# Kernel optimization log

Hardware: AMD Instinct MI355X
Metric: run time of the kernel (lower is better)

The kernel has to match this reference:

```python
import jax, jax.numpy as jnp
import numpy as np

K = 30  # hardcoded top-k in take_top_k_dropout(x, 30, ...)


def _topk_channel_mask(x, k):
    # x: [B, C, H, W]; binary mask with 1 at the top-k |x| channels per pixel.
    B, C, H, W = x.shape
    xa = jnp.abs(x).reshape(B, C, H * W).transpose(0, 2, 1).reshape(B * H * W, C)
    _, idx = jax.lax.top_k(xa, k)  # [BHW, k]
    rows = jnp.arange(B * H * W)[:, None]
    mask = jnp.zeros((B * H * W, C), x.dtype).at[rows, idx].set(1.0)
    return mask.reshape(B, H * W, C).transpose(0, 2, 1).reshape(B, C, H, W)


def _saturation(z, phi, jump):
    # Saturation_activation_per_filter.forward
    l1 = (jnp.sum(jnp.abs(phi), axis=0) + 1e-12).reshape(1, -1, 1, 1)  # [1,C,1,1]
    r = z / l1
    r = 0.5 * (jnp.sign(r - jump) + jnp.sign(r + jump))
    return r * l1


def _conv_transpose(x, w, b, stride):
    # PyTorch ConvTranspose2d(padding=0): w is [in, out, kh, kw]
    k = w.shape[-1]
    wt = jnp.flip(w, (2, 3)).transpose(1, 0, 2, 3)  # -> [out, in, kh, kw]
    y = jax.lax.conv_general_dilated(
        x, wt, window_strides=(1, 1),
        padding=[(k - 1, k - 1), (k - 1, k - 1)],
        lhs_dilation=(stride, stride),
        dimension_numbers=('NCHW', 'OIHW', 'NCHW'))
    return y + b.reshape(1, -1, 1, 1)


def _take_middle(x):
    width = x.shape[-1]
    s = (width - 32) // 2
    return x[:, :, s:s + 32, s:s + 32]


def setup_inputs() -> dict:
    key = jax.random.key(0)
    ks = jax.random.split(key, 9)
    B, C, H, W, D = 128, 500, 16, 16, 192
    return {
        'x': jax.random.normal(ks[0], (B, C, H, W), jnp.float32),
        'phi': jax.random.normal(ks[1], (D, C), jnp.float32),
        'jump': jnp.float32(0.1),
        'w1': jax.random.normal(ks[2], (C, 300, 4, 4), jnp.float32) * 0.02,
        'b1': jax.random.normal(ks[3], (300,), jnp.float32) * 0.02,
        'w2': jax.random.normal(ks[4], (300, 100, 3, 3), jnp.float32) * 0.02,
        'b2': jax.random.normal(ks[5], (100,), jnp.float32) * 0.02,
        'w3': jax.random.normal(ks[6], (100, 3, 3, 3), jnp.float32) * 0.02,
        'b3': jax.random.normal(ks[7], (3,), jnp.float32) * 0.02,
    }


def reference(x, phi, jump, w1, b1, w2, b2, w3, b3):
    # eval mode: dropout(ones) == ones, no training rescalings
    out = x * _topk_channel_mask(x, K)
    out = _saturation(out, phi, jump)
    out = jax.nn.relu(_conv_transpose(out, w1, b1, 2))
    out = jax.nn.relu(_conv_transpose(out, w2, b2, 1))
    out = jax.nn.relu(_conv_transpose(out, w3, b3, 1))
    return _take_middle(out)
```

## Files before the change

### kernel.cpp

```cpp
#include <hip/hip_runtime.h>
#include <stdint.h>

#define B_   128
#define C_   500
#define H_   16
#define P_   256
#define D_   192
#define C1O  300
#define H1   34
#define P1   (H1*H1)
#define C2O  100
#define H2   36
#define P2   (H2*H2)
#define C3O  3
#define H3   38
#define P3   (H3*H3)
#define CROP 3
#define OW_  32
#define KTOP 30

#define NL1B   16
#define NZQBLK (B_ * 4)
#define NB3BLK ((P3 + 3) / 4)

__device__ __forceinline__ float sgnf(float v){ return (v > 0.f) ? 1.f : ((v < 0.f) ? -1.f : 0.f); }

__device__ __forceinline__ int pat36(int i){
  if (i == 0) return 0;
  if (i == 1) return 1;
  if (i <= 33) return 2;
  if (i == 34) return 3;
  return 4;
}

__global__ void k_setup(const float* __restrict__ phi, const float* __restrict__ jumpp,
                        const float* __restrict__ w2, const float* __restrict__ b1,
                        const float* __restrict__ b2,
                        float* __restrict__ l1, float* __restrict__ thr,
                        float* __restrict__ tab, float4* __restrict__ zero_region){
  const int blk = blockIdx.x;
  const int t = threadIdx.x;

  if (blk >= NL1B + 100){
    const int idx0 = (blk - (NL1B + 100)) * 256 + t;
    const int nvec = (16 + B_ * P1 + B_ * P2) / 16;
    float4 z = make_float4(0.f, 0.f, 0.f, 0.f);
    for (int i = idx0; i < nvec; i += 64 * 256) zero_region[i] = z;
    return;
  }

  if (blk < NL1B){
    __shared__ float red[8][32];
    const int cl = t & 31, dg = t >> 5;
    const int c = blk * 32 + cl;
    float s = 0.f;
    if (c < C_){
      const int d0 = dg * 24;
#pragma unroll 4
      for (int d = d0; d < d0 + 24; ++d) s += fabsf(phi[d * C_ + c]);
    }
    red[dg][cl] = s;
    __syncthreads();
    if (t < 32){
      int cc = blk * 32 + t;
      if (cc < C_){
        float sum = 1e-12f;
#pragma unroll
        for (int g = 0; g < 8; ++g) sum += red[g][t];
        l1[cc] = sum;
        thr[cc] = jumpp[0] * sum;
      }
    }
    return;
  }

  __shared__ float S[9];
  const int o = blk - NL1B;
  if (t < 64){
    float acc[9] = {0,0,0,0,0,0,0,0,0};
    for (int c = t; c < C1O; c += 64){
      float a1 = fmaxf(b1[c], 0.f);
      const float* w = w2 + (c * C2O + o) * 9;
#pragma unroll
      for (int tap = 0; tap < 9; ++tap) acc[tap] += w[tap] * a1;
    }
#pragma unroll
    for (int tap = 0; tap < 9; ++tap)
      for (int off = 32; off; off >>= 1) acc[tap] += __shfl_down(acc[tap], off);
    if (t == 0){
#pragma unroll
      for (int tap = 0; tap < 9; ++tap) S[tap] = acc[tap];
    }
  }
  __syncthreads();
  if (t < 25){
    const int lo[5] = {0,0,0,1,2}, hi[5] = {0,1,2,2,2};
    int pr = t / 5, pc = t % 5;
    float s = b2[o];
    for (int kh = lo[pr]; kh <= hi[pr]; ++kh)
      for (int kw = lo[pc]; kw <= hi[pc]; ++kw) s += S[kh * 3 + kw];
    tab[o * 25 + t] = s;
  }
}

__global__ void k_zq_b3(const float* __restrict__ x, const float* __restrict__ l1,
                        const float* __restrict__ thr, const float* __restrict__ jumpp,
                        const float* __restrict__ tab, const float* __restrict__ w3,
                        const float* __restrict__ b3,
                        signed char* __restrict__ zq, unsigned char* __restrict__ d0,
                        float* __restrict__ base3, int* __restrict__ cnt){
  if (blockIdx.x >= NZQBLK){
    const int wave = threadIdx.x >> 6, lane = threadIdx.x & 63;
    const int pix = (blockIdx.x - NZQBLK) * 4 + wave;
    if (pix >= P3) return;
    const int oh = pix / H3, ow = pix % H3;
    float acc[3] = {0, 0, 0};
    for (int c = lane; c < C2O; c += 64){
      const float* w = w3 + c * 27;
#pragma unroll
      for (int kh = 0; kh < 3; ++kh){
        int ih = oh - kh; if (ih < 0 || ih >= H2) continue;
        int prr = pat36(ih) * 5;
#pragma unroll
        for (int kw = 0; kw < 3; ++kw){
          int iw = ow - kw; if (iw < 0 || iw >= H2) continue;
          float a2 = fmaxf(tab[c * 25 + prr + pat36(iw)], 0.f);
#pragma unroll
          for (int o = 0; o < 3; ++o) acc[o] += w[o * 9 + kh * 3 + kw] * a2;
        }
      }
    }
#pragma unroll
    for (int o = 0; o < 3; ++o){
      for (int off = 32; off; off >>= 1) acc[o] += __shfl_down(acc[o], off);
    }
    if (lane == 0){
#pragma unroll
      for (int o = 0; o < 3; ++o) base3[o * P3 + pix] = acc[o] + b3[o];
    }
    return;
  }

  const int b = blockIdx.x >> 2;
  const int tile = (blockIdx.x & 3) * 64;
  const int t = threadIdx.x;
  const int q = t & 15, cg = t >> 4;

  __shared__ unsigned char um[256];
  __shared__ unsigned char pixf[64];
  __shared__ int s_any;
  if (t == 0) s_any = 0;

  unsigned m = 0;
  const int pbase = tile + 4 * q;
  for (int c = cg; c < C_; c += 16){
    float tc = thr[c];
    const float4 v = *(const float4*)(x + ((size_t)(b * C_ + c)) * P_ + pbase);
    if (fabsf(v.x) >= tc) m |= 1u;
    if (fabsf(v.y) >= tc) m |= 2u;
    if (fabsf(v.z) >= tc) m |= 4u;
    if (fabsf(v.w) >= tc) m |= 8u;
  }
  um[t] = (unsigned char)m;
  __syncthreads();
  if (t < 16){
    unsigned mm = 0;
#pragma unroll
    for (int g = 0; g < 16; ++g) mm |= um[g * 16 + t];
#pragma unroll
    for (int j = 0; j < 4; ++j){
      unsigned char f = (unsigned char)((mm >> j) & 1u);
      pixf[4 * t + j] = f;
      d0[b * P_ + tile + 4 * t + j] = f;
    }
    if (mm) s_any = 1;
  }
  __syncthreads();
  if (t == 0 && s_any) atomicAdd(cnt, 1);
  if (!s_any) return;

  __shared__ float sx[C_];
  __shared__ unsigned char rm[C_];
  __shared__ unsigned long long red[4];
  __shared__ int sel[KTOP];
  float J = jumpp[0];
  for (int pp = 0; pp < 64; ++pp){
    if (!pixf[pp]) continue;
    int px = tile + pp;
    for (int c = t; c < C_; c += 256){ sx[c] = x[(b * C_ + c) * P_ + px]; rm[c] = 0; }
    __syncthreads();
    for (int it = 0; it < KTOP; ++it){
      unsigned long long best = 0ULL;
      for (int c = t; c < C_; c += 256){
        if (!rm[c]){
          unsigned long long key =
            ((unsigned long long)__float_as_uint(fabsf(sx[c])) << 32) |
            (unsigned int)(C_ - 1 - c);
          if (key > best) best = key;
        }
      }
      for (int off = 32; off; off >>= 1){
        unsigned long long o2 = __shfl_down(best, off);
        if (o2 > best) best = o2;
      }
      if ((t & 63) == 0) red[t >> 6] = best;
      __syncthreads();
      if (t == 0){
        unsigned long long mx = red[0];
        for (int wv = 1; wv < 4; ++wv) if (red[wv] > mx) mx = red[wv];
        int idx = C_ - 1 - (int)(mx & 0xffffffffULL);
        sel[it] = idx;
        rm[idx] = 1;
      }
      __syncthreads();
    }
    for (int c = t; c < C_; c += 256) zq[(b * C_ + c) * P_ + px] = 0;
    __syncthreads();
    if (t < KTOP){
      int c = sel[t];
      float z = sx[c];
      float r = z / l1[c];
      float qv = 0.5f * (sgnf(r - J) + sgnf(r + J));
      int code = (int)(2.f * qv);
      if (code) zq[(b * C_ + c) * P_ + px] = (signed char)code;
    }
    __syncthreads();
  }
}

__global__ void k_u1f(const signed char* __restrict__ zq, const float* __restrict__ l1,
                      const float* __restrict__ w1, const float* __restrict__ b1,
                      const unsigned char* __restrict__ d0, const int* __restrict__ cnt,
                      int* __restrict__ cnt1,
                      unsigned char* __restrict__ d1, float* __restrict__ u1, int have){
  if (cnt[0] == 0) return;
  const int wave = threadIdx.x >> 6, lane = threadIdx.x & 63;
  const int pix0 = (blockIdx.x * 4 + wave) * 64;
  const int tid = pix0 + lane;

  int b = tid / P1, p1 = tid - b * P1;
  int ih = p1 / H1, iw = p1 - ih * H1;
  int h0 = max(0, (ih - 2) >> 1), h1v = min(H_ - 1, ih >> 1);
  int w0 = max(0, (iw - 2) >> 1), w1v = min(H_ - 1, iw >> 1);
  int any = 0;
  for (int h = h0; h <= h1v; ++h)
    for (int w = w0; w <= w1v; ++w)
      any |= d0[b * P_ + h * H_ + w];
  unsigned long long mask = __ballot(any != 0);
  if (!mask) return;
  if (any) d1[tid] = 1;
  if (lane == 0) atomicAdd(cnt1, 1);

  while (mask){
    int pp = __ffsll((long long)mask) - 1;
    mask &= mask - 1;
    int pix = pix0 + pp;
    int bb = pix / P1, pq = pix - bb * P1;
    int oih = pq / H1, oiw = pq - oih * H1;
    float acc[5] = {0,0,0,0,0};
    int hh0 = max(0, (oih - 2) >> 1), hh1 = min(H_ - 1, oih >> 1);
    int ww0 = max(0, (oiw - 2) >> 1), ww1 = min(H_ - 1, oiw >> 1);
    for (int h = hh0; h <= hh1; ++h)
      for (int w = ww0; w <= ww1; ++w){
        if (!d0[bb * P_ + h * H_ + w]) continue;
        int kh = oih - 2 * h, kw = oiw - 2 * w;
        const signed char* zp = zq + (size_t)(bb * C_) * P_ + h * H_ + w;
        for (int c = 0; c < C_; ++c){
          int code = zp[(size_t)c * P_];
          if (!code) continue;
          float val = 0.5f * (float)code * l1[c];
          const float* wp = w1 + (size_t)(c * C1O) * 16 + kh * 4 + kw;
#pragma unroll
          for (int j = 0; j < 5; ++j){
            int c1 = j * 64 + lane;
            if (c1 < C1O) acc[j] += wp[(size_t)c1 * 16] * val;
          }
        }
      }
    if (have){
#pragma unroll
      for (int j = 0; j < 5; ++j){
        int c1 = j * 64 + lane;
        if (c1 < C1O){
          float bb1 = b1[c1];
          u1[(size_t)(bb * C1O + c1) * P1 + pq] = fmaxf(bb1 + acc[j], 0.f) - fmaxf(bb1, 0.f);
        }
      }
    }
  }
}

__global__ void k_u2f(const float* __restrict__ u1, const float* __restrict__ w2,
                      const float* __restrict__ tab, const unsigned char* __restrict__ d1,
                      const int* __restrict__ cnt1, int* __restrict__ cnt2,
                      unsigned char* __restrict__ d2, float* __restrict__ u2, int have){
  if (cnt1[0] == 0) return;
  const int wave = threadIdx.x >> 6, lane = threadIdx.x & 63;
  const int pix0 = (blockIdx.x * 4 + wave) * 64;
  const int tid = pix0 + lane;

  int b = tid / P2, p2 = tid - b * P2;
  int oh = p2 / H2, ow = p2 - oh * H2;
  int any = 0;
  for (int kh = 0; kh < 3; ++kh){
    int ih = oh - kh; if (ih < 0 || ih >= H1) continue;
    for (int kw = 0; kw < 3; ++kw){
      int iw = ow - kw; if (iw < 0 || iw >= H1) continue;
      any |= d1[b * P1 + ih * H1 + iw];
    }
  }
  unsigned long long mask = __ballot(any != 0);
  if (!mask) return;
  if (any) d2[tid] = 1;
  if (lane == 0) atomicAdd(cnt2, 1);

  while (mask){
    int pp = __ffsll((long long)mask) - 1;
    mask &= mask - 1;
    int pix = pix0 + pp;
    int bb = pix / P2, pq = pix - bb * P2;
    int ooh = pq / H2, oow = pq - ooh * H2;
    float acc[2] = {0,0};
    for (int kh = 0; kh < 3; ++kh){
      int ih = ooh - kh; if (ih < 0 || ih >= H1) continue;
      for (int kw = 0; kw < 3; ++kw){
        int iw = oow - kw; if (iw < 0 || iw >= H1) continue;
        if (!d1[bb * P1 + ih * H1 + iw]) continue;
        const float* up = u1 + (size_t)(bb * C1O) * P1 + ih * H1 + iw;
        const float* wb = w2 + kh * 3 + kw;
        for (int c1 = 0; c1 < C1O; ++c1){
          float uv = up[(size_t)c1 * P1];
          if (uv == 0.f) continue;
          const float* wp = wb + (size_t)(c1 * C2O) * 9;
#pragma unroll
          for (int j = 0; j < 2; ++j){
            int c2 = j * 64 + lane;
            if (c2 < C2O) acc[j] += wp[(size_t)c2 * 9] * uv;
          }
        }
      }
    }
    if (have){
      int pr = pat36(ooh) * 5 + pat36(oow);
#pragma unroll
      for (int j = 0; j < 2; ++j){
        int c2 = j * 64 + lane;
        if (c2 < C2O){
          float bs = tab[c2 * 25 + pr];
          u2[(size_t)(bb * C2O + c2) * P2 + pq] = fmaxf(bs + acc[j], 0.f) - fmaxf(bs, 0.f);
        }
      }
    }
  }
}

__global__ void k_out(const float* __restrict__ base3, const unsigned char* __restrict__ d2,
                      const float* __restrict__ u2, const float* __restrict__ w3,
                      const int* __restrict__ cnt2, float* __restrict__ out){
  int tid = blockIdx.x * blockDim.x + threadIdx.x;
  if (tid >= B_ * 3 * OW_ * (OW_ / 4)) return;
  const int perimg = 3 * OW_ * (OW_ / 4);
  int b = tid / perimg;
  int rem = tid - b * perimg;
  int o = rem >> 8;
  int rr = rem & 255;
  int r = rr >> 3, q4 = rr & 7;
  int oh = r + CROP;
  int ow0 = q4 * 4 + CROP;
  const float* bp = base3 + o * P3 + oh * H3 + ow0;

  float4 res;
  float* rp = &res.x;
  if (cnt2[0] == 0){
#pragma unroll
    for (int j = 0; j < 4; ++j) rp[j] = fmaxf(bp[j], 0.f);
  } else {
#pragma unroll
    for (int j = 0; j < 4; ++j){
      int ow = ow0 + j;
      float acc = bp[j];
      for (int kh = 0; kh < 3; ++kh){
        int ih = oh - kh;
        for (int kw = 0; kw < 3; ++kw){
          int iw = ow - kw;
          if (!d2[b * P2 + ih * H2 + iw]) continue;
          const float* up = u2 + (size_t)(b * C2O) * P2 + ih * H2 + iw;
          const float* wp = w3 + o * 9 + kh * 3 + kw;
          for (int c2 = 0; c2 < C2O; ++c2){
            float uv = up[(size_t)c2 * P2];
            if (uv != 0.f) acc += wp[c2 * 27] * uv;
          }
        }
      }
      rp[j] = fmaxf(acc, 0.f);
    }
  }
  *(float4*)(out + ((size_t)(b * 3 + o) * OW_ + r) * OW_ + q4 * 4) = res;
}

extern "C" void kernel_launch(void* const* d_in, const int* in_sizes, int n_in,
                              void* d_out, int out_size, void* d_ws, size_t ws_size,
                              hipStream_t stream){
  const float* x   = (const float*)d_in[0];
  const float* phi = (const float*)d_in[1];
  const float* jmp = (const float*)d_in[2];
  const float* w1  = (const float*)d_in[3];
  const float* b1  = (const float*)d_in[4];
  const float* w2  = (const float*)d_in[5];
  const float* b2  = (const float*)d_in[6];
  const float* w3  = (const float*)d_in[7];
  const float* b3  = (const float*)d_in[8];
  float* out = (float*)d_out;
  char* ws = (char*)d_ws;

  constexpr size_t OFF_L1  = 0;
  constexpr size_t OFF_THR = OFF_L1  + 2048;
  constexpr size_t OFF_TAB = OFF_THR + 2048;
  constexpr size_t OFF_B3  = OFF_TAB + 10240;
  constexpr size_t OFF_D0  = OFF_B3  + 17344;
  constexpr size_t OFF_CNT = OFF_D0  + (size_t)B_ * P_;
  constexpr size_t OFF_D1  = OFF_CNT + 16;
  constexpr size_t OFF_D2  = OFF_D1  + (size_t)B_ * P1;
  constexpr size_t OFF_ZQ  = OFF_D2  + (size_t)B_ * P2;
  constexpr size_t OFF_U1  = OFF_ZQ  + (size_t)B_ * C_ * P_;
  constexpr size_t OFF_U2  = OFF_U1  + (size_t)B_ * C1O * P1 * 4;
  constexpr size_t TOTAL   = OFF_U2  + (size_t)B_ * C2O * P2 * 4;

  float* l1p  = (float*)(ws + OFF_L1);
  float* thrp = (float*)(ws + OFF_THR);
  float* tabp = (float*)(ws + OFF_TAB);
  float* b3p  = (float*)(ws + OFF_B3);
  unsigned char* d0p = (unsigned char*)(ws + OFF_D0);
  int* cntp = (int*)(ws + OFF_CNT);
  unsigned char* d1p = (unsigned char*)(ws + OFF_D1);
  unsigned char* d2p = (unsigned char*)(ws + OFF_D2);
  signed char* zqp = (signed char*)(ws + OFF_ZQ);
  float* u1p = (float*)(ws + OFF_U1);
  float* u2p = (float*)(ws + OFF_U2);
  int have = (ws_size >= TOTAL) ? 1 : 0;

  k_setup<<<NL1B + 100 + 64, 256, 0, stream>>>(phi, jmp, w2, b1, b2,
                                               l1p, thrp, tabp, (float4*)cntp);
  k_zq_b3<<<NZQBLK + NB3BLK, 256, 0, stream>>>(x, l1p, thrp, jmp, tabp, w3, b3,
                                               zqp, d0p, b3p, cntp);
  k_u1f  <<<(B_ * P1) / 256, 256, 0, stream>>>(zqp, l1p, w1, b1, d0p, cntp, cntp + 1,
                                               d1p, u1p, have);
  k_u2f  <<<(B_ * P2) / 256, 256, 0, stream>>>(u1p, w2, tabp, d1p, cntp + 1, cntp + 2,
                                               d2p, u2p, have);
  k_out  <<<(B_ * 3 * OW_ * (OW_ / 4) + 255) / 256, 256, 0, stream>>>(
      b3p, d2p, u2p, w3, cntp + 2, out);
}
```

Baseline: 132.9 us.

## Fuse sparse top-k and deconv stages into one per-image kernel

Merges the top-k/quantize, first deconv, second deconv and output stages into a single kernel with one block per image. Dilation masks d1/d2 now live in shared memory instead of global memory, so the global zeroing pass and the atomic counters are no longer needed. The aim is to cut kernel launches and global memory traffic on the common path where no pixel is hot. The cost is that any image with hot pixels is handled serially by a single 256-thread block, which would be slow when the data is not sparse.

```diff
diff --git a/kernel.cpp b/kernel.cpp
--- a/kernel.cpp
+++ b/kernel.cpp
@@ -37,17 +37,9 @@
                         const float* __restrict__ w2, const float* __restrict__ b1,
                         const float* __restrict__ b2,
                         float* __restrict__ l1, float* __restrict__ thr,
-                        float* __restrict__ tab, float4* __restrict__ zero_region){
+                        float* __restrict__ tab){
   const int blk = blockIdx.x;
   const int t = threadIdx.x;
-
-  if (blk >= NL1B + 100){
-    const int idx0 = (blk - (NL1B + 100)) * 256 + t;
-    const int nvec = (16 + B_ * P1 + B_ * P2) / 16;
-    float4 z = make_float4(0.f, 0.f, 0.f, 0.f);
-    for (int i = idx0; i < nvec; i += 64 * 256) zero_region[i] = z;
-    return;
-  }
 
   if (blk < NL1B){
     __shared__ float red[8][32];
@@ -103,12 +95,10 @@
   }
 }
 
-__global__ void k_zq_b3(const float* __restrict__ x, const float* __restrict__ l1,
-                        const float* __restrict__ thr, const float* __restrict__ jumpp,
-                        const float* __restrict__ tab, const float* __restrict__ w3,
-                        const float* __restrict__ b3,
-                        signed char* __restrict__ zq, unsigned char* __restrict__ d0,
-                        float* __restrict__ base3, int* __restrict__ cnt){
+__global__ void k_scan_b3(const float* __restrict__ x, const float* __restrict__ thr,
+                          const float* __restrict__ tab, const float* __restrict__ w3,
+                          const float* __restrict__ b3,
+                          unsigned char* __restrict__ d0, float* __restrict__ base3){
   if (blockIdx.x >= NZQBLK){
     const int wave = threadIdx.x >> 6, lane = threadIdx.x & 63;
     const int pix = (blockIdx.x - NZQBLK) * 4 + wave;
@@ -147,9 +137,6 @@
   const int q = t & 15, cg = t >> 4;
 
   __shared__ unsigned char um[256];
-  __shared__ unsigned char pixf[64];
-  __shared__ int s_any;
-  if (t == 0) s_any = 0;
 
   unsigned m = 0;
   const int pbase = tile + 4 * q;
@@ -163,30 +150,62 @@
   }
   um[t] = (unsigned char)m;
   __syncthreads();
-  if (t < 16){
+  if (t < 64){
+    const int qq = t >> 2, j = t & 3;
     unsigned mm = 0;
 #pragma unroll
-    for (int g = 0; g < 16; ++g) mm |= um[g * 16 + t];
-#pragma unroll
-    for (int j = 0; j < 4; ++j){
-      unsigned char f = (unsigned char)((mm >> j) & 1u);
-      pixf[4 * t + j] = f;
-      d0[b * P_ + tile + 4 * t + j] = f;
-    }
-    if (mm) s_any = 1;
-  }
-  __syncthreads();
-  if (t == 0 && s_any) atomicAdd(cnt, 1);
-  if (!s_any) return;
-
+    for (int g = 0; g < 16; ++g) mm |= um[g * 16 + qq];
+    d0[b * P_ + tile + t] = (unsigned char)((mm >> j) & 1u);
+  }
+}
+
+__global__ void k_final(const float* __restrict__ x, const float* __restrict__ l1,
+                        const float* __restrict__ jumpp, const float* __restrict__ tab,
+                        const float* __restrict__ w1, const float* __restrict__ b1,
+                        const float* __restrict__ w2, const float* __restrict__ w3,
+                        const float* __restrict__ base3, const unsigned char* __restrict__ d0,
+                        signed char* __restrict__ zq, float* __restrict__ u1,
+                        float* __restrict__ u2, float* __restrict__ out, int have){
+  const int b = blockIdx.x;
+  const int t = threadIdx.x;
+  const int wave = t >> 6, lane = t & 63;
+
+  __shared__ unsigned char hot[P_];
+  __shared__ unsigned char d1s[P1];
+  __shared__ unsigned char d2s[P2];
+  __shared__ int s_any;
   __shared__ float sx[C_];
   __shared__ unsigned char rm[C_];
   __shared__ unsigned long long red[4];
   __shared__ int sel[KTOP];
-  float J = jumpp[0];
-  for (int pp = 0; pp < 64; ++pp){
-    if (!pixf[pp]) continue;
-    int px = tile + pp;
+
+  hot[t] = d0[b * P_ + t];
+  if (t == 0) s_any = 0;
+  __syncthreads();
+  if (hot[t]) s_any = 1;
+  __syncthreads();
+
+  if (!s_any){
+    for (int i = t; i < 3 * OW_ * (OW_ / 4); i += 256){
+      int o = i >> 8, rr = i & 255;
+      int r = rr >> 3, q4 = rr & 7;
+      int oh = r + CROP, ow0 = q4 * 4 + CROP;
+      const float* bp = base3 + o * P3 + oh * H3 + ow0;
+      float4 res;
+      res.x = fmaxf(bp[0], 0.f);
+      res.y = fmaxf(bp[1], 0.f);
+      res.z = fmaxf(bp[2], 0.f);
+      res.w = fmaxf(bp[3], 0.f);
+      *(float4*)(out + ((size_t)(b * 3 + o) * OW_ + r) * OW_ + q4 * 4) = res;
+    }
+    return;
+  }
+  if (!have) return;
+
+  const float J = jumpp[0];
+
+  for (int px = 0; px < P_; ++px){
+    if (!hot[px]) continue;
     for (int c = t; c < C_; c += 256){ sx[c] = x[(b * C_ + c) * P_ + px]; rm[c] = 0; }
     __syncthreads();
     for (int it = 0; it < KTOP; ++it){
@@ -218,53 +237,51 @@
     __syncthreads();
     if (t < KTOP){
       int c = sel[t];
-      float z = sx[c];
-      float r = z / l1[c];
+      float r = sx[c] / l1[c];
       float qv = 0.5f * (sgnf(r - J) + sgnf(r + J));
       int code = (int)(2.f * qv);
       if (code) zq[(b * C_ + c) * P_ + px] = (signed char)code;
     }
     __syncthreads();
   }
-}
-
-__global__ void k_u1f(const signed char* __restrict__ zq, const float* __restrict__ l1,
-                      const float* __restrict__ w1, const float* __restrict__ b1,
-                      const unsigned char* __restrict__ d0, const int* __restrict__ cnt,
-                      int* __restrict__ cnt1,
-                      unsigned char* __restrict__ d1, float* __restrict__ u1, int have){
-  if (cnt[0] == 0) return;
-  const int wave = threadIdx.x >> 6, lane = threadIdx.x & 63;
-  const int pix0 = (blockIdx.x * 4 + wave) * 64;
-  const int tid = pix0 + lane;
-
-  int b = tid / P1, p1 = tid - b * P1;
-  int ih = p1 / H1, iw = p1 - ih * H1;
-  int h0 = max(0, (ih - 2) >> 1), h1v = min(H_ - 1, ih >> 1);
-  int w0 = max(0, (iw - 2) >> 1), w1v = min(H_ - 1, iw >> 1);
-  int any = 0;
-  for (int h = h0; h <= h1v; ++h)
-    for (int w = w0; w <= w1v; ++w)
-      any |= d0[b * P_ + h * H_ + w];
-  unsigned long long mask = __ballot(any != 0);
-  if (!mask) return;
-  if (any) d1[tid] = 1;
-  if (lane == 0) atomicAdd(cnt1, 1);
-
-  while (mask){
-    int pp = __ffsll((long long)mask) - 1;
-    mask &= mask - 1;
-    int pix = pix0 + pp;
-    int bb = pix / P1, pq = pix - bb * P1;
-    int oih = pq / H1, oiw = pq - oih * H1;
+
+  for (int p1 = t; p1 < P1; p1 += 256){
+    int ih = p1 / H1, iw = p1 - (p1 / H1) * H1;
+    int h0 = max(0, (ih - 2) >> 1), h1v = min(H_ - 1, ih >> 1);
+    int w0 = max(0, (iw - 2) >> 1), w1v = min(H_ - 1, iw >> 1);
+    int any = 0;
+    for (int h = h0; h <= h1v; ++h)
+      for (int w = w0; w <= w1v; ++w)
+        any |= hot[h * H_ + w];
+    d1s[p1] = (unsigned char)(any != 0);
+  }
+  __syncthreads();
+
+  for (int p2 = t; p2 < P2; p2 += 256){
+    int oh = p2 / H2, ow = p2 - (p2 / H2) * H2;
+    int any = 0;
+    for (int kh = 0; kh < 3; ++kh){
+      int ih = oh - kh; if (ih < 0 || ih >= H1) continue;
+      for (int kw = 0; kw < 3; ++kw){
+        int iw = ow - kw; if (iw < 0 || iw >= H1) continue;
+        any |= d1s[ih * H1 + iw];
+      }
+    }
+    d2s[p2] = (unsigned char)(any != 0);
+  }
+  __syncthreads();
+
+  for (int p1 = wave; p1 < P1; p1 += 4){
+    if (!d1s[p1]) continue;
+    int ih = p1 / H1, iw = p1 - (p1 / H1) * H1;
     float acc[5] = {0,0,0,0,0};
-    int hh0 = max(0, (oih - 2) >> 1), hh1 = min(H_ - 1, oih >> 1);
-    int ww0 = max(0, (oiw - 2) >> 1), ww1 = min(H_ - 1, oiw >> 1);
-    for (int h = hh0; h <= hh1; ++h)
-      for (int w = ww0; w <= ww1; ++w){
-        if (!d0[bb * P_ + h * H_ + w]) continue;
-        int kh = oih - 2 * h, kw = oiw - 2 * w;
-        const signed char* zp = zq + (size_t)(bb * C_) * P_ + h * H_ + w;
+    int h0 = max(0, (ih - 2) >> 1), h1v = min(H_ - 1, ih >> 1);
+    int w0 = max(0, (iw - 2) >> 1), w1v = min(H_ - 1, iw >> 1);
+    for (int h = h0; h <= h1v; ++h)
+      for (int w = w0; w <= w1v; ++w){
+        if (!hot[h * H_ + w]) continue;
+        int kh = ih - 2 * h, kw = iw - 2 * w;
+        const signed char* zp = zq + (size_t)(b * C_) * P_ + h * H_ + w;
         for (int c = 0; c < C_; ++c){
           int code = zp[(size_t)c * P_];
           if (!code) continue;
@@ -277,56 +294,27 @@
           }
         }
       }
-    if (have){
-#pragma unroll
-      for (int j = 0; j < 5; ++j){
-        int c1 = j * 64 + lane;
-        if (c1 < C1O){
-          float bb1 = b1[c1];
-          u1[(size_t)(bb * C1O + c1) * P1 + pq] = fmaxf(bb1 + acc[j], 0.f) - fmaxf(bb1, 0.f);
-        }
-      }
-    }
-  }
-}
-
-__global__ void k_u2f(const float* __restrict__ u1, const float* __restrict__ w2,
-                      const float* __restrict__ tab, const unsigned char* __restrict__ d1,
-                      const int* __restrict__ cnt1, int* __restrict__ cnt2,
-                      unsigned char* __restrict__ d2, float* __restrict__ u2, int have){
-  if (cnt1[0] == 0) return;
-  const int wave = threadIdx.x >> 6, lane = threadIdx.x & 63;
-  const int pix0 = (blockIdx.x * 4 + wave) * 64;
-  const int tid = pix0 + lane;
-
-  int b = tid / P2, p2 = tid - b * P2;
-  int oh = p2 / H2, ow = p2 - oh * H2;
-  int any = 0;
-  for (int kh = 0; kh < 3; ++kh){
-    int ih = oh - kh; if (ih < 0 || ih >= H1) continue;
-    for (int kw = 0; kw < 3; ++kw){
-      int iw = ow - kw; if (iw < 0 || iw >= H1) continue;
-      any |= d1[b * P1 + ih * H1 + iw];
-    }
-  }
-  unsigned long long mask = __ballot(any != 0);
-  if (!mask) return;
-  if (any) d2[tid] = 1;
-  if (lane == 0) atomicAdd(cnt2, 1);
-
-  while (mask){
-    int pp = __ffsll((long long)mask) - 1;
-    mask &= mask - 1;
-    int pix = pix0 + pp;
-    int bb = pix / P2, pq = pix - bb * P2;
-    int ooh = pq / H2, oow = pq - ooh * H2;
+#pragma unroll
+    for (int j = 0; j < 5; ++j){
+      int c1 = j * 64 + lane;
+      if (c1 < C1O){
+        float bb = b1[c1];
+        u1[(size_t)(b * C1O + c1) * P1 + p1] = fmaxf(bb + acc[j], 0.f) - fmaxf(bb, 0.f);
+      }
+    }
+  }
+  __syncthreads();
+
+  for (int p2 = wave; p2 < P2; p2 += 4){
+    if (!d2s[p2]) continue;
+    int oh = p2 / H2, ow = p2 - (p2 / H2) * H2;
     float acc[2] = {0,0};
     for (int kh = 0; kh < 3; ++kh){
-      int ih = ooh - kh; if (ih < 0 || ih >= H1) continue;
+      int ih = oh - kh; if (ih < 0 || ih >= H1) continue;
       for (int kw = 0; kw < 3; ++kw){
-        int iw = oow - kw; if (iw < 0 || iw >= H1) continue;
-        if (!d1[bb * P1 + ih * H1 + iw]) continue;
-        const float* up = u1 + (size_t)(bb * C1O) * P1 + ih * H1 + iw;
+        int iw = ow - kw; if (iw < 0 || iw >= H1) continue;
+        if (!d1s[ih * H1 + iw]) continue;
+        const float* up = u1 + (size_t)(b * C1O) * P1 + ih * H1 + iw;
         const float* wb = w2 + kh * 3 + kw;
         for (int c1 = 0; c1 < C1O; ++c1){
           float uv = up[(size_t)c1 * P1];
@@ -340,62 +328,38 @@
         }
       }
     }
-    if (have){
-      int pr = pat36(ooh) * 5 + pat36(oow);
-#pragma unroll
-      for (int j = 0; j < 2; ++j){
-        int c2 = j * 64 + lane;
-        if (c2 < C2O){
-          float bs = tab[c2 * 25 + pr];
-          u2[(size_t)(bb * C2O + c2) * P2 + pq] = fmaxf(bs + acc[j], 0.f) - fmaxf(bs, 0.f);
+    int pr = pat36(oh) * 5 + pat36(ow);
+#pragma unroll
+    for (int j = 0; j < 2; ++j){
+      int c2 = j * 64 + lane;
+      if (c2 < C2O){
+        float bs = tab[c2 * 25 + pr];
+        u2[(size_t)(b * C2O + c2) * P2 + p2] = fmaxf(bs + acc[j], 0.f) - fmaxf(bs, 0.f);
+      }
+    }
+  }
+  __syncthreads();
+
+  for (int i = t; i < 3 * OW_ * OW_; i += 256){
+    int o = i >> 10, rc = i & 1023;
+    int r = rc >> 5, cc = rc & 31;
+    int oh = r + CROP, ow = cc + CROP;
+    float acc = base3[o * P3 + oh * H3 + ow];
+    for (int kh = 0; kh < 3; ++kh){
+      int ih = oh - kh;
+      for (int kw = 0; kw < 3; ++kw){
+        int iw = ow - kw;
+        if (!d2s[ih * H2 + iw]) continue;
+        const float* up = u2 + (size_t)(b * C2O) * P2 + ih * H2 + iw;
+        const float* wp = w3 + o * 9 + kh * 3 + kw;
+        for (int c2 = 0; c2 < C2O; ++c2){
+          float uv = up[(size_t)c2 * P2];
+          if (uv != 0.f) acc += wp[c2 * 27] * uv;
         }
       }
     }
-  }
-}
-
-__global__ void k_out(const float* __restrict__ base3, const unsigned char* __restrict__ d2,
-                      const float* __restrict__ u2, const float* __restrict__ w3,
-                      const int* __restrict__ cnt2, float* __restrict__ out){
-  int tid = blockIdx.x * blockDim.x + threadIdx.x;
-  if (tid >= B_ * 3 * OW_ * (OW_ / 4)) return;
-  const int perimg = 3 * OW_ * (OW_ / 4);
-  int b = tid / perimg;
-  int rem = tid - b * perimg;
-  int o = rem >> 8;
-  int rr = rem & 255;
-  int r = rr >> 3, q4 = rr & 7;
-  int oh = r + CROP;
-  int ow0 = q4 * 4 + CROP;
-  const float* bp = base3 + o * P3 + oh * H3 + ow0;
-
-  float4 res;
-  float* rp = &res.x;
-  if (cnt2[0] == 0){
-#pragma unroll
-    for (int j = 0; j < 4; ++j) rp[j] = fmaxf(bp[j], 0.f);
-  } else {
-#pragma unroll
-    for (int j = 0; j < 4; ++j){
-      int ow = ow0 + j;
-      float acc = bp[j];
-      for (int kh = 0; kh < 3; ++kh){
-        int ih = oh - kh;
-        for (int kw = 0; kw < 3; ++kw){
-          int iw = ow - kw;
-          if (!d2[b * P2 + ih * H2 + iw]) continue;
-          const float* up = u2 + (size_t)(b * C2O) * P2 + ih * H2 + iw;
-          const float* wp = w3 + o * 9 + kh * 3 + kw;
-          for (int c2 = 0; c2 < C2O; ++c2){
-            float uv = up[(size_t)c2 * P2];
-            if (uv != 0.f) acc += wp[c2 * 27] * uv;
-          }
-        }
-      }
-      rp[j] = fmaxf(acc, 0.f);
-    }
-  }
-  *(float4*)(out + ((size_t)(b * 3 + o) * OW_ + r) * OW_ + q4 * 4) = res;
+    out[((size_t)(b * 3 + o) * OW_ + r) * OW_ + cc] = fmaxf(acc, 0.f);
+  }
 }
 
 extern "C" void kernel_launch(void* const* d_in, const int* in_sizes, int n_in,
@@ -418,10 +382,7 @@
   constexpr size_t OFF_TAB = OFF_THR + 2048;
   constexpr size_t OFF_B3  = OFF_TAB + 10240;
   constexpr size_t OFF_D0  = OFF_B3  + 17344;
-  constexpr size_t OFF_CNT = OFF_D0  + (size_t)B_ * P_;
-  constexpr size_t OFF_D1  = OFF_CNT + 16;
-  constexpr size_t OFF_D2  = OFF_D1  + (size_t)B_ * P1;
-  constexpr size_t OFF_ZQ  = OFF_D2  + (size_t)B_ * P2;
+  constexpr size_t OFF_ZQ  = OFF_D0  + (size_t)B_ * P_;
   constexpr size_t OFF_U1  = OFF_ZQ  + (size_t)B_ * C_ * P_;
   constexpr size_t OFF_U2  = OFF_U1  + (size_t)B_ * C1O * P1 * 4;
   constexpr size_t TOTAL   = OFF_U2  + (size_t)B_ * C2O * P2 * 4;
@@ -431,22 +392,13 @@
   float* tabp = (float*)(ws + OFF_TAB);
   float* b3p  = (float*)(ws + OFF_B3);
   unsigned char* d0p = (unsigned char*)(ws + OFF_D0);
-  int* cntp = (int*)(ws + OFF_CNT);
-  unsigned char* d1p = (unsigned char*)(ws + OFF_D1);
-  unsigned char* d2p = (unsigned char*)(ws + OFF_D2);
   signed char* zqp = (signed char*)(ws + OFF_ZQ);
   float* u1p = (float*)(ws + OFF_U1);
   float* u2p = (float*)(ws + OFF_U2);
   int have = (ws_size >= TOTAL) ? 1 : 0;
 
-  k_setup<<<NL1B + 100 + 64, 256, 0, stream>>>(phi, jmp, w2, b1, b2,
-                                               l1p, thrp, tabp, (float4*)cntp);
-  k_zq_b3<<<NZQBLK + NB3BLK, 256, 0, stream>>>(x, l1p, thrp, jmp, tabp, w3, b3,
-                                               zqp, d0p, b3p, cntp);
-  k_u1f  <<<(B_ * P1) / 256, 256, 0, stream>>>(zqp, l1p, w1, b1, d0p, cntp, cntp + 1,
-                                               d1p, u1p, have);
-  k_u2f  <<<(B_ * P2) / 256, 256, 0, stream>>>(u1p, w2, tabp, d1p, cntp + 1, cntp + 2,
-                                               d2p, u2p, have);
-  k_out  <<<(B_ * 3 * OW_ * (OW_ / 4) + 255) / 256, 256, 0, stream>>>(
-      b3p, d2p, u2p, w3, cntp + 2, out);
+  k_setup  <<<NL1B + 100, 256, 0, stream>>>(phi, jmp, w2, b1, b2, l1p, thrp, tabp);
+  k_scan_b3<<<NZQBLK + NB3BLK, 256, 0, stream>>>(x, thrp, tabp, w3, b3, d0p, b3p);
+  k_final  <<<B_, 256, 0, stream>>>(x, l1p, jmp, tabp, w1, b1, w2, w3,
+                                    b3p, d0p, zqp, u1p, u2p, out, have);
 }
```

After: 129.6 us. 2.5% less time.
